# Optimization experiments

Hardware: AMD Instinct MI355X
Metric: run time of the kernel (lower is better)

The kernel has to match this reference:

```python
import jax, jax.numpy as jnp
import numpy as np

N, E, G = 50000, 800000, 64
H, C, EDIM = 4, 64, 16
NT, NR, NCLS = 8, 6, 2
NEG_SLOPE = 0.2


def setup_inputs() -> dict:
    key = jax.random.key(0)
    ks = jax.random.split(key, 24)
    d = {}
    d['node_type'] = jax.random.randint(ks[0], (N,), 0, NT, dtype=jnp.int32)
    d['edge_type'] = jax.random.randint(ks[1], (E,), 0, NR, dtype=jnp.int32)
    d['edge_index'] = jax.random.randint(ks[2], (2, E), 0, N, dtype=jnp.int32)
    d['batch'] = jnp.sort(jax.random.randint(ks[3], (N,), 0, G, dtype=jnp.int32))
    i = [4]
    def rn(shape, scale=0.1):
        a = jax.random.normal(ks[i[0]], shape, dtype=jnp.float32) * scale
        i[0] += 1
        return a
    d['node_emb'] = rn((NT, C))
    d['edge_emb'] = rn((NR, EDIM))
    for l in (0, 1):
        d[f'W{l}'] = rn((C, H * C))
        d[f'We{l}'] = rn((EDIM, H * C))
        d[f'att_src{l}'] = rn((H, C))
        d[f'att_dst{l}'] = rn((H, C))
        d[f'att_edge{l}'] = rn((H, C))
        d[f'b{l}'] = jnp.zeros((C,), jnp.float32)
    d['cw1'] = rn((C, C))
    d['cb1'] = jnp.zeros((C,), jnp.float32)
    d['cw2'] = rn((C, NCLS))
    d['cb2'] = jnp.zeros((NCLS,), jnp.float32)
    return d


def gat_layer(x, ea, src, dst, W, We, a_src, a_dst, a_edge, b):
    # x: [N, C], ea: [E, EDIM]
    h = (x @ W).reshape(N, H, C)          # transformed node features
    he = (ea @ We).reshape(E, H, C)       # transformed edge features
    # per-edge attention logits [E, H]
    alpha = ((h * a_src).sum(-1)[src]
             + (h * a_dst).sum(-1)[dst]
             + (he * a_edge).sum(-1))
    alpha = jax.nn.leaky_relu(alpha, NEG_SLOPE)
    # segment softmax over destination neighborhoods
    m = jax.ops.segment_max(alpha, dst, num_segments=N)
    alpha = jnp.exp(alpha - m[dst])
    den = jax.ops.segment_sum(alpha, dst, num_segments=N)
    alpha = alpha / (den[dst] + 1e-16)
    # weighted scatter-add of source features, then mean over heads
    out = jax.ops.segment_sum(alpha[:, :, None] * h[src], dst, num_segments=N)
    return jax.nn.elu(out.mean(axis=1) + b)


def reference(node_type, edge_type, edge_index, batch, node_emb, edge_emb,
              W0, We0, att_src0, att_dst0, att_edge0, b0,
              W1, We1, att_src1, att_dst1, att_edge1, b1,
              cw1, cb1, cw2, cb2):
    src, dst = edge_index[0], edge_index[1]
    x = node_emb[node_type]          # [N, C]
    ea = edge_emb[edge_type]         # [E, EDIM]
    x = gat_layer(x, ea, src, dst, W0, We0, att_src0, att_dst0, att_edge0, b0)
    x = gat_layer(x, ea, src, dst, W1, We1, att_src1, att_dst1, att_edge1, b1)
    # global mean pool over graphs
    s = jax.ops.segment_sum(x, batch, num_segments=G)
    cnt = jax.ops.segment_sum(jnp.ones((N, 1), x.dtype), batch, num_segments=G)
    g = s / jnp.maximum(cnt, 1.0)
    # classifier (dropout inactive in eval)
    return jax.nn.relu(g @ cw1 + cb1) @ cw2 + cb2
```

## Files before the change

### kernel.cpp

```cpp
#include <hip/hip_runtime.h>
#include <hip/hip_bf16.h>

#define N_NODES 50000
#define N_EDGES 800000
#define N_GRAPH 64
#define NHEAD 4
#define CDIM 64
#define HC 256
#define NTT 8
#define NRR 6
#define EDIMM 16
#define SCAN_CHUNK 1024
#define NBLK_SCAN ((N_NODES + SCAN_CHUNK - 1) / SCAN_CHUNK)
#define H1SCALE 1024.f

typedef unsigned short u16;
typedef unsigned char u8;
typedef __attribute__((ext_vector_type(8))) short bf8;
typedef __attribute__((ext_vector_type(4))) float f4;
typedef __attribute__((ext_vector_type(2))) float v2f;

__device__ __forceinline__ float eluf(float v) { return v > 0.f ? v : expm1f(v); }
__device__ __forceinline__ u16 f2u(float f) {
    union { float f; unsigned int i; } c; c.f = f;
    unsigned int i = c.i;
    return (u16)((i + 0x7FFFu + ((i >> 16) & 1u)) >> 16);
}
__device__ __forceinline__ float lrelu(float v) { return v > 0.f ? v : 0.2f * v; }
__device__ __forceinline__ u8 f2fp8(float v) {
    return (u8)(__builtin_amdgcn_cvt_pk_fp8_f32(v, 0.f, 0, false) & 0xFF);
}

__global__ __launch_bounds__(256) void k_zero(float* __restrict__ p, int n)
{
    int i = blockIdx.x * 256 + threadIdx.x;
    if (i < n) p[i] = 0.f;
}

__global__ __launch_bounds__(256) void k_tables(
    const float* __restrict__ node_emb, const float* __restrict__ edge_emb,
    const float* __restrict__ W0, const float* __restrict__ We0,
    const float* __restrict__ as0, const float* __restrict__ ad0,
    const float* __restrict__ ae0, const float* __restrict__ We1,
    const float* __restrict__ ae1,
    float* __restrict__ t_h0, float* __restrict__ t_as0,
    float* __restrict__ t_ad0, float* __restrict__ t_ae0,
    float* __restrict__ t_ae1)
{
    __shared__ float srow[HC];
    __shared__ float srow2[HC];
    int tid = threadIdx.x;
    int b = blockIdx.x;
    if (b < NTT) {
        int t = b;
        float acc = 0.f;
        #pragma unroll 8
        for (int k = 0; k < CDIM; k++)
            acc += node_emb[t * CDIM + k] * W0[k * HC + tid];
        srow[tid] = acc;
        t_h0[t * HC + tid] = acc;
        __syncthreads();
        if (tid < NHEAD) {
            int h = tid;
            float a = 0.f, d = 0.f;
            for (int c = 0; c < CDIM; c++) {
                float hv = srow[h * CDIM + c];
                a += hv * as0[h * CDIM + c];
                d += hv * ad0[h * CDIM + c];
            }
            t_as0[t * NHEAD + h] = a;
            t_ad0[t * NHEAD + h] = d;
        }
    } else {
        int r = b - NTT;
        float a0 = 0.f, a1 = 0.f;
        #pragma unroll
        for (int k = 0; k < EDIMM; k++) {
            float ev = edge_emb[r * EDIMM + k];
            a0 += ev * We0[k * HC + tid];
            a1 += ev * We1[k * HC + tid];
        }
        srow[tid] = a0;
        srow2[tid] = a1;
        __syncthreads();
        if (tid < NHEAD) {
            int h = tid;
            float s0 = 0.f, s1 = 0.f;
            for (int c = 0; c < CDIM; c++) {
                s0 += srow[h * CDIM + c] * ae0[h * CDIM + c];
                s1 += srow2[h * CDIM + c] * ae1[h * CDIM + c];
            }
            t_ae0[r * NHEAD + h] = s0;
            t_ae1[r * NHEAD + h] = s1;
        }
    }
}

__global__ __launch_bounds__(256) void k_exptab(
    const float* __restrict__ t_as0, const float* __restrict__ t_ad0,
    const float* __restrict__ t_ae0, float* __restrict__ t_exp)
{
    for (int idx = threadIdx.x; idx < NTT * NRR * NTT * NHEAD; idx += 256) {
        int tn = idx / 192;
        int rem = idx - tn * 192;
        int et = rem >> 5;
        int ts = (rem >> 2) & 7;
        int h = rem & 3;
        float lg = t_as0[ts * NHEAD + h] + t_ad0[tn * NHEAD + h]
                 + t_ae0[et * NHEAD + h];
        t_exp[idx] = __expf(lrelu(lg));
    }
}

__global__ __launch_bounds__(256) void k_count(
    const int* __restrict__ edge_index, int* __restrict__ deg4,
    const int* __restrict__ batch, int* __restrict__ goffs)
{
    int i = blockIdx.x * 256 + threadIdx.x;
    if (i < N_EDGES)
        atomicAdd(&deg4[(blockIdx.x & 3) * N_NODES + edge_index[N_EDGES + i]], 1);
    if (i < N_NODES) {
        int bi = batch[i];
        int bp = (i == 0) ? -1 : batch[i - 1];
        for (int g = bp + 1; g <= bi; g++) goffs[g] = i;
        if (i == N_NODES - 1)
            for (int g = bi + 1; g <= N_GRAPH; g++) goffs[g] = N_NODES;
    }
}

__global__ __launch_bounds__(256) void k_scan1(
    const int* __restrict__ deg4, int* __restrict__ deg, int* __restrict__ blksum)
{
    __shared__ int s[256];
    int b = blockIdx.x, tid = threadIdx.x;
    int base = b * SCAN_CHUNK + tid * 4;
    int t = 0;
    #pragma unroll
    for (int k = 0; k < 4; k++) {
        int i = base + k;
        if (i < N_NODES) {
            int d = deg4[i] + deg4[N_NODES + i] + deg4[2 * N_NODES + i]
                  + deg4[3 * N_NODES + i];
            deg[i] = d;
            t += d;
        }
    }
    s[tid] = t;
    __syncthreads();
    for (int off = 128; off > 0; off >>= 1) {
        if (tid < off) s[tid] += s[tid + off];
        __syncthreads();
    }
    if (tid == 0) blksum[b] = s[0];
}

__global__ __launch_bounds__(256) void k_scan3(
    const int* __restrict__ deg, const int* __restrict__ blksum,
    int* __restrict__ offs, int* __restrict__ cursor)
{
    __shared__ int s[256];
    __shared__ int sbase;
    int b = blockIdx.x, tid = threadIdx.x;
    if (tid < 64) {
        int v = (tid < b) ? blksum[tid] : 0;
        #pragma unroll
        for (int d = 32; d >= 1; d >>= 1) v += __shfl_xor(v, d);
        if (tid == 0) sbase = v;
    }
    int base = b * SCAN_CHUNK + tid * 4;
    int d4[4]; int t = 0;
    #pragma unroll
    for (int k = 0; k < 4; k++) {
        int i = base + k;
        d4[k] = (i < N_NODES) ? deg[i] : 0;
        t += d4[k];
    }
    s[tid] = t;
    __syncthreads();
    for (int off = 1; off < 256; off <<= 1) {
        int v = (tid >= off) ? s[tid - off] : 0;
        __syncthreads();
        s[tid] += v;
        __syncthreads();
    }
    int excl = sbase + s[tid] - t;
    #pragma unroll
    for (int k = 0; k < 4; k++) {
        int i = base + k;
        if (i < N_NODES) { offs[i] = excl; cursor[i] = excl; }
        excl += d4[k];
    }
    if (b == NBLK_SCAN - 1 && tid == 255) offs[N_NODES] = excl;
}

__global__ __launch_bounds__(256) void k_scatter(
    const int* __restrict__ edge_index, const int* __restrict__ edge_type,
    const int* __restrict__ node_type, int* __restrict__ cursor,
    int* __restrict__ csrp)
{
    int e = blockIdx.x * 256 + threadIdx.x;
    if (e < N_EDGES) {
        int d  = edge_index[N_EDGES + e];
        int s  = edge_index[e];
        int et = edge_type[e];
        int ts = node_type[s];
        int pos = atomicAdd(&cursor[d], 1);
        csrp[pos] = s | (et << 16) | (ts << 19);
    }
}

__global__ __launch_bounds__(256) void k_layer0(
    const int* __restrict__ node_type, const int* __restrict__ offs,
    const int* __restrict__ csrp,
    const float* __restrict__ t_h0, const float* __restrict__ t_exp,
    const float* __restrict__ b0, u16* __restrict__ x1b)
{
    __shared__ float s_h0[NTT * HC];
    __shared__ float s_exp[NTT * NRR * NTT * NHEAD];
    __shared__ float s_b0[CDIM];

    int tid = threadIdx.x;
    for (int i = tid; i < NTT * HC; i += 256) s_h0[i] = t_h0[i];
    for (int i = tid; i < NTT * NRR * NTT * NHEAD; i += 256) s_exp[i] = t_exp[i];
    if (tid < CDIM) s_b0[tid] = b0[tid];
    __syncthreads();

    int n = (blockIdx.x * 256 + tid) >> 6;
    int lane = tid & 63;
    int h = lane >> 4;
    int cq = (lane & 15) << 2;
    int hoff = h * CDIM + cq;

    int tnbase = node_type[n] * 192 + h;
    int e0 = offs[n], e1 = offs[n + 1];
    int efull = e0 + ((e1 - e0) & ~3);
    float ax = 0.f, ay = 0.f, az = 0.f, aw = 0.f, den = 0.f;
    for (int i = e0; i < efull; i += 4) {
        int rA = csrp[i],     rB = csrp[i + 1];
        int rC = csrp[i + 2], rD = csrp[i + 3];
        int tA = rA >> 19, tB = rB >> 19, tC = rC >> 19, tD = rD >> 19;
        int eA = (rA >> 16) & 7, eB = (rB >> 16) & 7;
        int eC = (rC >> 16) & 7, eD = (rD >> 16) & 7;
        float pA = s_exp[tnbase + (eA << 5) + (tA << 2)];
        float pB = s_exp[tnbase + (eB << 5) + (tB << 2)];
        float pC = s_exp[tnbase + (eC << 5) + (tC << 2)];
        float pD = s_exp[tnbase + (eD << 5) + (tD << 2)];
        den += pA + pB + pC + pD;
        const float4 vA = *(const float4*)(s_h0 + tA * HC + hoff);
        const float4 vB = *(const float4*)(s_h0 + tB * HC + hoff);
        const float4 vC = *(const float4*)(s_h0 + tC * HC + hoff);
        const float4 vD = *(const float4*)(s_h0 + tD * HC + hoff);
        ax += pA * vA.x + pB * vB.x + pC * vC.x + pD * vD.x;
        ay += pA * vA.y + pB * vB.y + pC * vC.y + pD * vD.y;
        az += pA * vA.z + pB * vB.z + pC * vC.z + pD * vD.z;
        aw += pA * vA.w + pB * vB.w + pC * vC.w + pD * vD.w;
    }
    for (int i = efull; i < e1; i++) {
        int r = csrp[i];
        int ts = r >> 19, et = (r >> 16) & 7;
        float p = s_exp[tnbase + (et << 5) + (ts << 2)];
        den += p;
        const float4 v = *(const float4*)(s_h0 + ts * HC + hoff);
        ax += p * v.x; ay += p * v.y; az += p * v.z; aw += p * v.w;
    }
    float inv = 0.25f / (den + 1e-16f);
    ax *= inv; ay *= inv; az *= inv; aw *= inv;
    ax += __shfl_xor(ax, 16); ax += __shfl_xor(ax, 32);
    ay += __shfl_xor(ay, 16); ay += __shfl_xor(ay, 32);
    az += __shfl_xor(az, 16); az += __shfl_xor(az, 32);
    aw += __shfl_xor(aw, 16); aw += __shfl_xor(aw, 32);
    if (lane < 16) {
        ushort4 o;
        o.x = f2u(eluf(ax + s_b0[cq + 0]));
        o.y = f2u(eluf(ay + s_b0[cq + 1]));
        o.z = f2u(eluf(az + s_b0[cq + 2]));
        o.w = f2u(eluf(aw + s_b0[cq + 3]));
        *(ushort4*)(x1b + (size_t)n * CDIM + cq) = o;
    }
}

__global__ __launch_bounds__(256) void k_gemm1(
    const u16* __restrict__ x1b, const float* __restrict__ W1,
    const float* __restrict__ as1, const float* __restrict__ ad1,
    u8* __restrict__ h1f8, float* __restrict__ asrc1, float* __restrict__ adst1)
{
    __shared__ u8 ht[16 * HC];
    int tid = threadIdx.x;
    int lane = tid & 63, wv = tid >> 6;
    int quad = lane >> 4, c16 = lane & 15;

    bf8 bf[4][2];
    float sv[4], dv[4];
    #pragma unroll
    for (int t = 0; t < 4; t++) {
        int col = wv * 64 + t * 16 + c16;
        sv[t] = as1[col];
        dv[t] = ad1[col];
        #pragma unroll
        for (int kf = 0; kf < 2; kf++)
            #pragma unroll
            for (int j = 0; j < 8; j++)
                bf[t][kf][j] = (short)f2u(W1[(kf * 32 + quad * 8 + j) * HC + col]);
    }

    for (int it = 0; it < 5; it++) {
        int nt = it * 625 + blockIdx.x;
        const bf8 a0 = *(const bf8*)(x1b + (size_t)(nt * 16 + c16) * CDIM + quad * 8);
        const bf8 a1 = *(const bf8*)(x1b + (size_t)(nt * 16 + c16) * CDIM + 32 + quad * 8);
        f4 acc[4];
        #pragma unroll
        for (int t = 0; t < 4; t++) {
            acc[t] = (f4){0.f, 0.f, 0.f, 0.f};
            acc[t] = __builtin_amdgcn_mfma_f32_16x16x32_bf16(a0, bf[t][0], acc[t], 0, 0, 0);
            acc[t] = __builtin_amdgcn_mfma_f32_16x16x32_bf16(a1, bf[t][1], acc[t], 0, 0, 0);
        }
        float rs[4] = {0.f, 0.f, 0.f, 0.f}, rd[4] = {0.f, 0.f, 0.f, 0.f};
        #pragma unroll
        for (int t = 0; t < 4; t++)
            #pragma unroll
            for (int reg = 0; reg < 4; reg++) {
                float v = acc[t][reg];
                rs[reg] += v * sv[t];
                rd[reg] += v * dv[t];
                ht[(quad * 4 + reg) * HC + wv * 64 + t * 16 + c16] = f2fp8(v * H1SCALE);
            }
        #pragma unroll
        for (int reg = 0; reg < 4; reg++)
            #pragma unroll
            for (int d = 1; d < 16; d <<= 1) {
                rs[reg] += __shfl_xor(rs[reg], d);
                rd[reg] += __shfl_xor(rd[reg], d);
            }
        if (c16 == 0) {
            #pragma unroll
            for (int reg = 0; reg < 4; reg++) {
                int n = nt * 16 + quad * 4 + reg;
                asrc1[n * NHEAD + wv] = rs[reg];
                adst1[n * NHEAD + wv] = rd[reg];
            }
        }
        __syncthreads();
        const uint4* src = (const uint4*)ht;
        uint4* dst = (uint4*)(h1f8 + (size_t)nt * 16 * HC);
        dst[tid] = src[tid];
        __syncthreads();
    }
}

__global__ __launch_bounds__(256) void k_agg1(
    const int* __restrict__ offs, const int* __restrict__ csrp,
    const u8* __restrict__ h1f8, const float* __restrict__ asrc1,
    const float* __restrict__ adst1, const float* __restrict__ t_ae1,
    const float* __restrict__ b1, float* __restrict__ x2)
{
    __shared__ float s_ae[NRR * NHEAD];
    if (threadIdx.x < NRR * NHEAD) s_ae[threadIdx.x] = t_ae1[threadIdx.x];
    __syncthreads();

    int n = (blockIdx.x * 256 + threadIdx.x) >> 6;
    int lane = threadIdx.x & 63;
    int h = lane >> 4;
    int cq = (lane & 15) << 2;
    float adst = adst1[n * NHEAD + h];
    int e0 = offs[n], e1 = offs[n + 1];
    int efull = e0 + ((e1 - e0) & ~7);

    float ax = 0.f, ay = 0.f, az = 0.f, aw = 0.f, den = 0.f;
    for (int i = e0; i < efull; i += 8) {
        int rec[8], s[8], et[8];
        #pragma unroll
        for (int k = 0; k < 8; k++) rec[k] = csrp[i + k];
        #pragma unroll
        for (int k = 0; k < 8; k++) { s[k] = rec[k] & 0xFFFF; et[k] = (rec[k] >> 16) & 7; }
        float asv[8];
        unsigned int hw[8];
        #pragma unroll
        for (int k = 0; k < 8; k++) asv[k] = asrc1[s[k] * NHEAD + h];
        #pragma unroll
        for (int k = 0; k < 8; k++)
            hw[k] = *(const unsigned int*)(h1f8 + (size_t)s[k] * HC + h * CDIM + cq);
        #pragma unroll
        for (int k = 0; k < 8; k++) {
            float p = __expf(lrelu(asv[k] + adst + s_ae[et[k] * NHEAD + h]));
            den += p;
            v2f lo = __builtin_amdgcn_cvt_pk_f32_fp8(hw[k], false);
            v2f hi = __builtin_amdgcn_cvt_pk_f32_fp8(hw[k], true);
            ax += p * lo.x; ay += p * lo.y;
            az += p * hi.x; aw += p * hi.y;
        }
    }
    for (int i = efull; i < e1; i++) {
        int rec = csrp[i];
        int s = rec & 0xFFFF, et = (rec >> 16) & 7;
        float p = __expf(lrelu(asrc1[s * NHEAD + h] + adst + s_ae[et * NHEAD + h]));
        den += p;
        unsigned int w = *(const unsigned int*)(h1f8 + (size_t)s * HC + h * CDIM + cq);
        v2f lo = __builtin_amdgcn_cvt_pk_f32_fp8(w, false);
        v2f hi = __builtin_amdgcn_cvt_pk_f32_fp8(w, true);
        ax += p * lo.x; ay += p * lo.y;
        az += p * hi.x; aw += p * hi.y;
    }
    float inv = (0.25f / H1SCALE) / (den + 1e-16f);
    ax *= inv; ay *= inv; az *= inv; aw *= inv;
    ax += __shfl_xor(ax, 16); ax += __shfl_xor(ax, 32);
    ay += __shfl_xor(ay, 16); ay += __shfl_xor(ay, 32);
    az += __shfl_xor(az, 16); az += __shfl_xor(az, 32);
    aw += __shfl_xor(aw, 16); aw += __shfl_xor(aw, 32);
    if (lane < 16) {
        float4 o;
        o.x = eluf(ax + b1[cq + 0]);
        o.y = eluf(ay + b1[cq + 1]);
        o.z = eluf(az + b1[cq + 2]);
        o.w = eluf(aw + b1[cq + 3]);
        *(float4*)(x2 + (size_t)n * CDIM + cq) = o;
    }
}

__global__ __launch_bounds__(256) void k_poolcls(
    const float* __restrict__ x2, const int* __restrict__ goffs,
    const float* __restrict__ cw1, const float* __restrict__ cb1,
    const float* __restrict__ cw2, const float* __restrict__ cb2,
    float* __restrict__ out, int wsMB,
    const int* __restrict__ offs, const int* __restrict__ csrp,
    const float* __restrict__ W1)
{
    __shared__ float part[4][CDIM];
    __shared__ float gsh[CDIM];
    int g = blockIdx.x;
    int ch = threadIdx.x & 63, rg = threadIdx.x >> 6;
    int gs = goffs[g], ge = goffs[g + 1];
    float acc = 0.f;
    for (int r = gs + rg; r < ge; r += 4)
        acc += x2[(size_t)r * CDIM + ch];
    part[rg][ch] = acc;
    __syncthreads();
    if (threadIdx.x < CDIM) {
        float s = part[0][ch] + part[1][ch] + part[2][ch] + part[3][ch];
        int c = ge - gs;
        gsh[ch] = s / (float)(c > 1 ? c : 1);
    }
    __syncthreads();
    if (threadIdx.x < 64) {
        int j = threadIdx.x;
        float a = cb1[j];
        #pragma unroll
        for (int k = 0; k < CDIM; k++) a += gsh[k] * cw1[k * CDIM + j];
        float hid = a > 0.f ? a : 0.f;
        float o0 = hid * cw2[j * 2 + 0];
        float o1 = hid * cw2[j * 2 + 1];
        #pragma unroll
        for (int d = 32; d >= 1; d >>= 1) {
            o0 += __shfl_xor(o0, d);
            o1 += __shfl_xor(o1, d);
        }
        if (j == 0) {
            out[g * 2 + 0] = o0 + cb2[0];
            out[g * 2 + 1] = o1 + cb2[1];
        }
    }
    if (g == 0) {
        __shared__ int simpl, soob, sA;
        if (threadIdx.x == 0) { simpl = 0; soob = 0; sA = 0; }
        __syncthreads();
        if (threadIdx.x == 0 && offs[N_NODES] != N_EDGES) atomicOr(&sA, 4);
        float v = W1[threadIdx.x];
        if (!(fabsf(v) < 100.f)) atomicAdd(&simpl, 1);
        int r = csrp[threadIdx.x];
        if ((r & 0xFFFF) >= N_NODES || (r >> 22) != 0 || r < 0) atomicAdd(&soob, 1);
        __syncthreads();
        if (threadIdx.x == 0) {
            int A = sA;
            if (simpl > 10) A |= 8;
            int B = soob > 1023 ? 1023 : soob;
            if (A | B) out[0] = (float)((A << 20) | (wsMB << 10) | B);
        }
    }
}

__global__ void k_fault(int code, float* __restrict__ out)
{
    if (threadIdx.x == 0 && blockIdx.x == 0) out[0] = (float)code;
}

extern "C" void kernel_launch(void* const* d_in, const int* in_sizes, int n_in,
                              void* d_out, int out_size, void* d_ws, size_t ws_size,
                              hipStream_t stream) {
    static const int rsize[22] = {50000, 800000, 1600000, 50000, 512, 96,
                                  16384, 4096, 256, 256, 256, 64,
                                  16384, 4096, 256, 256, 256, 64,
                                  4096, 64, 128, 2};
    static const int cand_pos[3][22] = {
        {21,19,18,12,20,17,0,2,8,4,6,10,1,3,9,5,7,11,15,13,16,14},
        {0,1,2,3,4,5,6,7,8,9,10,11,12,13,14,15,16,17,18,19,20,21},
        {17,15,14,8,16,13,18,20,4,0,2,6,19,21,5,1,3,7,11,9,12,10},
    };
    int mc = -1;
    if (n_in == 22) {
        for (int c = 0; c < 3 && mc < 0; c++) {
            bool ok = true;
            for (int r = 0; r < 22; r++)
                if (in_sizes[cand_pos[c][r]] != rsize[r]) { ok = false; break; }
            if (ok) mc = c;
        }
    }

    char* ws = (char*)d_ws;
    size_t off = 0;
    auto alloc = [&](size_t b) { size_t r = off; off += (b + 255) & ~(size_t)255; return r; };
    int*   deg4   = (int*)(ws + alloc((size_t)4 * N_NODES * 4));
    size_t zero_bytes = off;
    int*   deg    = (int*)(ws + alloc(N_NODES * 4));
    int*   blksum = (int*)(ws + alloc(NBLK_SCAN * 4));
    int*   offs   = (int*)(ws + alloc((N_NODES + 1) * 4));
    int*   cursor = (int*)(ws + alloc(N_NODES * 4));
    int*   csrp   = (int*)(ws + alloc(N_EDGES * 4));
    int*   goffs  = (int*)(ws + alloc((N_GRAPH + 1) * 4));
    float* t_h0   = (float*)(ws + alloc(NTT * HC * 4));
    float* t_as0  = (float*)(ws + alloc(NTT * NHEAD * 4));
    float* t_ad0  = (float*)(ws + alloc(NTT * NHEAD * 4));
    float* t_ae0  = (float*)(ws + alloc(NRR * NHEAD * 4));
    float* t_ae1  = (float*)(ws + alloc(NRR * NHEAD * 4));
    float* t_exp  = (float*)(ws + alloc(NTT * NRR * NTT * NHEAD * 4));
    u16*   x1b    = (u16*)(ws + alloc((size_t)N_NODES * CDIM * 2));
    float* asrc1  = (float*)(ws + alloc((size_t)N_NODES * NHEAD * 4));
    float* adst1  = (float*)(ws + alloc((size_t)N_NODES * NHEAD * 4));
    u8*    h1f8   = (u8*)(ws + alloc((size_t)N_NODES * HC));
    float* x2     = (float*)(ws + alloc((size_t)N_NODES * CDIM * 4));

    int wsMB = (int)(ws_size >> 20); if (wsMB > 1023) wsMB = 1023;
    int hostA = 0, hostB = 0;
    if (mc < 0) { hostA |= 1; hostB = (n_in != 22) ? (n_in < 1023 ? n_in : 1023) : 0; }
    if (mc >= 0 && off > ws_size) hostA |= 2;

    if (hostA == 0) {
        const int* P = cand_pos[mc];
        const int*   node_type  = (const int*)d_in[P[0]];
        const int*   edge_type  = (const int*)d_in[P[1]];
        const int*   edge_index = (const int*)d_in[P[2]];
        const int*   batch      = (const int*)d_in[P[3]];
        const float* node_emb   = (const float*)d_in[P[4]];
        const float* edge_emb   = (const float*)d_in[P[5]];
        const float* W0  = (const float*)d_in[P[6]];
        const float* We0 = (const float*)d_in[P[7]];
        const float* as0 = (const float*)d_in[P[8]];
        const float* ad0 = (const float*)d_in[P[9]];
        const float* ae0 = (const float*)d_in[P[10]];
        const float* b0  = (const float*)d_in[P[11]];
        const float* W1  = (const float*)d_in[P[12]];
        const float* We1 = (const float*)d_in[P[13]];
        const float* as1 = (const float*)d_in[P[14]];
        const float* ad1 = (const float*)d_in[P[15]];
        const float* ae1 = (const float*)d_in[P[16]];
        const float* b1  = (const float*)d_in[P[17]];
        const float* cw1 = (const float*)d_in[P[18]];
        const float* cb1 = (const float*)d_in[P[19]];
        const float* cw2 = (const float*)d_in[P[20]];
        const float* cb2 = (const float*)d_in[P[21]];

        int zero_elems = (int)(zero_bytes / 4);
        k_zero<<<(zero_elems + 255) / 256, 256, 0, stream>>>((float*)ws, zero_elems);
        k_tables<<<NTT + NRR, 256, 0, stream>>>(node_emb, edge_emb, W0, We0, as0,
                                                ad0, ae0, We1, ae1,
                                                t_h0, t_as0, t_ad0, t_ae0, t_ae1);
        k_exptab<<<1, 256, 0, stream>>>(t_as0, t_ad0, t_ae0, t_exp);
        k_count<<<(N_EDGES + 255) / 256, 256, 0, stream>>>(edge_index, deg4,
                                                           batch, goffs);
        k_scan1<<<NBLK_SCAN, 256, 0, stream>>>(deg4, deg, blksum);
        k_scan3<<<NBLK_SCAN, 256, 0, stream>>>(deg, blksum, offs, cursor);
        k_scatter<<<(N_EDGES + 255) / 256, 256, 0, stream>>>(edge_index, edge_type,
                                                             node_type, cursor, csrp);
        k_layer0<<<(N_NODES * 64) / 256, 256, 0, stream>>>(
            node_type, offs, csrp, t_h0, t_exp, b0, x1b);
        k_gemm1<<<625, 256, 0, stream>>>(
            x1b, W1, as1, ad1, h1f8, asrc1, adst1);
        k_agg1<<<(N_NODES * 64) / 256, 256, 0, stream>>>(
            offs, csrp, h1f8, asrc1, adst1, t_ae1, b1, x2);
        k_poolcls<<<N_GRAPH, 256, 0, stream>>>(
            x2, goffs, cw1, cb1, cw2, cb2, (float*)d_out, wsMB, offs, csrp, W1);
    } else {
        int code = (hostA << 20) | (wsMB << 10) | (hostB > 1023 ? 1023 : hostB);
        k_fault<<<1, 64, 0, stream>>>(code, (float*)d_out);
    }
}
```

Baseline: 347.9 us.

## Bin layer0 by source type and precompute layer1 edge attention weights

Layer 0 now splits each node's edges across lanes that accumulate attention weight per source node type. It then runs an 8-term weighted sum over the type table instead of a per-edge feature gather. For layer 1, a new per-edge kernel computes the exponentiated attention logits once for all four heads into a buffer, so the aggregation kernel no longer does a scattered asrc gather and exp per head-lane. This adds a destination-index array, an extra 12.8MB edge buffer write/read and one more kernel launch. The exptab head index is also changed to idx&3, which is the same value as before since 192 is a multiple of 4.

```diff
diff --git a/kernel.cpp b/kernel.cpp
--- a/kernel.cpp
+++ b/kernel.cpp
@@ -105,7 +105,7 @@
         int rem = idx - tn * 192;
         int et = rem >> 5;
         int ts = (rem >> 2) & 7;
-        int h = rem & 3;
+        int h = idx & 3;
         float lg = t_as0[ts * NHEAD + h] + t_ad0[tn * NHEAD + h]
                  + t_ae0[et * NHEAD + h];
         t_exp[idx] = __expf(lrelu(lg));
@@ -196,7 +196,7 @@
 __global__ __launch_bounds__(256) void k_scatter(
     const int* __restrict__ edge_index, const int* __restrict__ edge_type,
     const int* __restrict__ node_type, int* __restrict__ cursor,
-    int* __restrict__ csrp)
+    int* __restrict__ csrp, int* __restrict__ csrd)
 {
     int e = blockIdx.x * 256 + threadIdx.x;
     if (e < N_EDGES) {
@@ -206,7 +206,31 @@
         int ts = node_type[s];
         int pos = atomicAdd(&cursor[d], 1);
         csrp[pos] = s | (et << 16) | (ts << 19);
-    }
+        csrd[pos] = d;
+    }
+}
+
+__global__ __launch_bounds__(256) void k_edgep(
+    const int* __restrict__ csrp, const int* __restrict__ csrd,
+    const float* __restrict__ asrc1, const float* __restrict__ adst1,
+    const float* __restrict__ t_ae1, float* __restrict__ pbuf)
+{
+    __shared__ float s_ae[NRR * NHEAD];
+    if (threadIdx.x < NRR * NHEAD) s_ae[threadIdx.x] = t_ae1[threadIdx.x];
+    __syncthreads();
+    int i = blockIdx.x * 256 + threadIdx.x;
+    if (i >= N_EDGES) return;
+    int rec = csrp[i];
+    int s = rec & 0xFFFF, et = (rec >> 16) & 7;
+    int d = csrd[i];
+    const float4 a4 = *(const float4*)(asrc1 + (size_t)s * NHEAD);
+    const float4 b4 = *(const float4*)(adst1 + (size_t)d * NHEAD);
+    float4 p;
+    p.x = __expf(lrelu(a4.x + b4.x + s_ae[et * NHEAD + 0]));
+    p.y = __expf(lrelu(a4.y + b4.y + s_ae[et * NHEAD + 1]));
+    p.z = __expf(lrelu(a4.z + b4.z + s_ae[et * NHEAD + 2]));
+    p.w = __expf(lrelu(a4.w + b4.w + s_ae[et * NHEAD + 3]));
+    *(float4*)(pbuf + (size_t)i * NHEAD) = p;
 }
 
 __global__ __launch_bounds__(256) void k_layer0(
@@ -227,41 +251,32 @@
 
     int n = (blockIdx.x * 256 + tid) >> 6;
     int lane = tid & 63;
-    int h = lane >> 4;
+
+    int j   = lane & 1;
+    int hE  = (lane >> 1) & 3;
+    int tsp = (lane >> 3) & 7;
+    int tn = node_type[n];
+    int pbase = tn * 192 + tsp * 4 + hE;
+    int e0 = offs[n], e1 = offs[n + 1];
+    float w = 0.f;
+    for (int i = e0 + j; i < e1; i += 2) {
+        int rec = csrp[i];
+        int ts = rec >> 19, et = (rec >> 16) & 7;
+        float p = s_exp[pbase + (et << 5)];
+        w += (ts == tsp) ? p : 0.f;
+    }
+    w += __shfl_xor(w, 1);
+
+    int h2 = lane >> 4;
     int cq = (lane & 15) << 2;
-    int hoff = h * CDIM + cq;
-
-    int tnbase = node_type[n] * 192 + h;
-    int e0 = offs[n], e1 = offs[n + 1];
-    int efull = e0 + ((e1 - e0) & ~3);
+    int hoff = h2 * CDIM + cq;
     float ax = 0.f, ay = 0.f, az = 0.f, aw = 0.f, den = 0.f;
-    for (int i = e0; i < efull; i += 4) {
-        int rA = csrp[i],     rB = csrp[i + 1];
-        int rC = csrp[i + 2], rD = csrp[i + 3];
-        int tA = rA >> 19, tB = rB >> 19, tC = rC >> 19, tD = rD >> 19;
-        int eA = (rA >> 16) & 7, eB = (rB >> 16) & 7;
-        int eC = (rC >> 16) & 7, eD = (rD >> 16) & 7;
-        float pA = s_exp[tnbase + (eA << 5) + (tA << 2)];
-        float pB = s_exp[tnbase + (eB << 5) + (tB << 2)];
-        float pC = s_exp[tnbase + (eC << 5) + (tC << 2)];
-        float pD = s_exp[tnbase + (eD << 5) + (tD << 2)];
-        den += pA + pB + pC + pD;
-        const float4 vA = *(const float4*)(s_h0 + tA * HC + hoff);
-        const float4 vB = *(const float4*)(s_h0 + tB * HC + hoff);
-        const float4 vC = *(const float4*)(s_h0 + tC * HC + hoff);
-        const float4 vD = *(const float4*)(s_h0 + tD * HC + hoff);
-        ax += pA * vA.x + pB * vB.x + pC * vC.x + pD * vD.x;
-        ay += pA * vA.y + pB * vB.y + pC * vC.y + pD * vD.y;
-        az += pA * vA.z + pB * vB.z + pC * vC.z + pD * vD.z;
-        aw += pA * vA.w + pB * vB.w + pC * vC.w + pD * vD.w;
-    }
-    for (int i = efull; i < e1; i++) {
-        int r = csrp[i];
-        int ts = r >> 19, et = (r >> 16) & 7;
-        float p = s_exp[tnbase + (et << 5) + (ts << 2)];
-        den += p;
+    #pragma unroll
+    for (int ts = 0; ts < NTT; ts++) {
+        float wt = __shfl(w, ts * 8 + h2 * 2);
+        den += wt;
         const float4 v = *(const float4*)(s_h0 + ts * HC + hoff);
-        ax += p * v.x; ay += p * v.y; az += p * v.z; aw += p * v.w;
+        ax += wt * v.x; ay += wt * v.y; az += wt * v.z; aw += wt * v.w;
     }
     float inv = 0.25f / (den + 1e-16f);
     ax *= inv; ay *= inv; az *= inv; aw *= inv;
@@ -349,39 +364,31 @@
 
 __global__ __launch_bounds__(256) void k_agg1(
     const int* __restrict__ offs, const int* __restrict__ csrp,
-    const u8* __restrict__ h1f8, const float* __restrict__ asrc1,
-    const float* __restrict__ adst1, const float* __restrict__ t_ae1,
+    const u8* __restrict__ h1f8, const float* __restrict__ pbuf,
     const float* __restrict__ b1, float* __restrict__ x2)
 {
-    __shared__ float s_ae[NRR * NHEAD];
-    if (threadIdx.x < NRR * NHEAD) s_ae[threadIdx.x] = t_ae1[threadIdx.x];
-    __syncthreads();
-
     int n = (blockIdx.x * 256 + threadIdx.x) >> 6;
     int lane = threadIdx.x & 63;
     int h = lane >> 4;
     int cq = (lane & 15) << 2;
-    float adst = adst1[n * NHEAD + h];
     int e0 = offs[n], e1 = offs[n + 1];
     int efull = e0 + ((e1 - e0) & ~7);
 
     float ax = 0.f, ay = 0.f, az = 0.f, aw = 0.f, den = 0.f;
     for (int i = e0; i < efull; i += 8) {
-        int rec[8], s[8], et[8];
-        #pragma unroll
-        for (int k = 0; k < 8; k++) rec[k] = csrp[i + k];
-        #pragma unroll
-        for (int k = 0; k < 8; k++) { s[k] = rec[k] & 0xFFFF; et[k] = (rec[k] >> 16) & 7; }
-        float asv[8];
+        int s[8];
+        float pv[8];
         unsigned int hw[8];
         #pragma unroll
-        for (int k = 0; k < 8; k++) asv[k] = asrc1[s[k] * NHEAD + h];
+        for (int k = 0; k < 8; k++) s[k] = csrp[i + k] & 0xFFFF;
+        #pragma unroll
+        for (int k = 0; k < 8; k++) pv[k] = pbuf[(size_t)(i + k) * NHEAD + h];
         #pragma unroll
         for (int k = 0; k < 8; k++)
             hw[k] = *(const unsigned int*)(h1f8 + (size_t)s[k] * HC + h * CDIM + cq);
         #pragma unroll
         for (int k = 0; k < 8; k++) {
-            float p = __expf(lrelu(asv[k] + adst + s_ae[et[k] * NHEAD + h]));
+            float p = pv[k];
             den += p;
             v2f lo = __builtin_amdgcn_cvt_pk_f32_fp8(hw[k], false);
             v2f hi = __builtin_amdgcn_cvt_pk_f32_fp8(hw[k], true);
@@ -390,9 +397,8 @@
         }
     }
     for (int i = efull; i < e1; i++) {
-        int rec = csrp[i];
-        int s = rec & 0xFFFF, et = (rec >> 16) & 7;
-        float p = __expf(lrelu(asrc1[s * NHEAD + h] + adst + s_ae[et * NHEAD + h]));
+        int s = csrp[i] & 0xFFFF;
+        float p = pbuf[(size_t)i * NHEAD + h];
         den += p;
         unsigned int w = *(const unsigned int*)(h1f8 + (size_t)s * HC + h * CDIM + cq);
         v2f lo = __builtin_amdgcn_cvt_pk_f32_fp8(w, false);
@@ -514,6 +520,7 @@
     int*   offs   = (int*)(ws + alloc((N_NODES + 1) * 4));
     int*   cursor = (int*)(ws + alloc(N_NODES * 4));
     int*   csrp   = (int*)(ws + alloc(N_EDGES * 4));
+    int*   csrd   = (int*)(ws + alloc(N_EDGES * 4));
     int*   goffs  = (int*)(ws + alloc((N_GRAPH + 1) * 4));
     float* t_h0   = (float*)(ws + alloc(NTT * HC * 4));
     float* t_as0  = (float*)(ws + alloc(NTT * NHEAD * 4));
@@ -525,6 +532,7 @@
     float* asrc1  = (float*)(ws + alloc((size_t)N_NODES * NHEAD * 4));
     float* adst1  = (float*)(ws + alloc((size_t)N_NODES * NHEAD * 4));
     u8*    h1f8   = (u8*)(ws + alloc((size_t)N_NODES * HC));
+    float* pbuf   = (float*)(ws + alloc((size_t)N_EDGES * NHEAD * 4));
     float* x2     = (float*)(ws + alloc((size_t)N_NODES * CDIM * 4));
 
     int wsMB = (int)(ws_size >> 20); if (wsMB > 1023) wsMB = 1023;
@@ -568,13 +576,16 @@
         k_scan1<<<NBLK_SCAN, 256, 0, stream>>>(deg4, deg, blksum);
         k_scan3<<<NBLK_SCAN, 256, 0, stream>>>(deg, blksum, offs, cursor);
         k_scatter<<<(N_EDGES + 255) / 256, 256, 0, stream>>>(edge_index, edge_type,
-                                                             node_type, cursor, csrp);
+                                                             node_type, cursor,
+                                                             csrp, csrd);
         k_layer0<<<(N_NODES * 64) / 256, 256, 0, stream>>>(
             node_type, offs, csrp, t_h0, t_exp, b0, x1b);
         k_gemm1<<<625, 256, 0, stream>>>(
             x1b, W1, as1, ad1, h1f8, asrc1, adst1);
+        k_edgep<<<(N_EDGES + 255) / 256, 256, 0, stream>>>(
+            csrp, csrd, asrc1, adst1, t_ae1, pbuf);
         k_agg1<<<(N_NODES * 64) / 256, 256, 0, stream>>>(
-            offs, csrp, h1f8, asrc1, adst1, t_ae1, b1, x2);
+            offs, csrp, h1f8, pbuf, b1, x2);
         k_poolcls<<<N_GRAPH, 256, 0, stream>>>(
             x2, goffs, cw1, cb1, cw2, cb2, (float*)d_out, wsMB, offs, csrp, W1);
     } else {
```

After: 358.2 us. 1.03x slower.
